# Optimization experiments

Measured on AMD Instinct MI355X. Metric: run time of the kernel, lower is better.

Reference implementation:

```python
import jax, jax.numpy as jnp
import numpy as np

N_NODES = 50000
N_EDGES = 600000
F_IN = 128
F_OUT = 128


def setup_inputs() -> dict:
    key = jax.random.key(0)
    k1, k2, k3, k4, k5 = jax.random.split(key, 5)
    x = jax.random.normal(k1, (N_NODES, F_IN), dtype=jnp.float32)
    src = jax.random.randint(k2, (N_EDGES,), 0, N_NODES)
    dst = jax.random.randint(k3, (N_EDGES,), 0, N_NODES)
    scale = 1.0 / np.sqrt(F_IN).astype(np.float32)
    W_self = jax.random.normal(k4, (F_IN, F_OUT), dtype=jnp.float32) * scale
    W_neigh = jax.random.normal(k5, (F_IN, F_OUT), dtype=jnp.float32) * scale
    b = jnp.zeros((F_OUT,), dtype=jnp.float32)
    return {"x": x, "W_self": W_self, "W_neigh": W_neigh, "b": b, "src": src, "dst": dst}


def reference(x, W_self, W_neigh, b, src, dst):
    # DGL SAGEConv, aggregator_type='mean':
    #   h_neigh[v] = mean_{(u->v) in E} x[u]   (0 for zero in-degree nodes)
    #   out = relu(x @ W_self + h_neigh @ W_neigh + b)
    msgs = x[src]  # [E, F_IN] gather of source features
    agg = jax.ops.segment_sum(msgs, dst, num_segments=N_NODES)  # [N, F_IN]
    deg = jax.ops.segment_sum(jnp.ones((src.shape[0],), x.dtype), dst,
                              num_segments=N_NODES)  # [N]
    h_neigh = agg / jnp.maximum(deg, 1.0)[:, None]  # zero-degree -> 0
    out = x @ W_self + h_neigh @ W_neigh + b
    return jax.nn.relu(out)
```

## Files before the change

### kernel.cpp

```cpp
#include <hip/hip_runtime.h>

#define F 128
#define HP 136
#define CAP 62
#define RSTR 64
#define PBASE ((int)0xAAAAAAAA)

typedef short bf16x8 __attribute__((ext_vector_type(8)));
typedef float f32x4  __attribute__((ext_vector_type(4)));

__device__ __forceinline__ unsigned short f2bf(float f) {
    unsigned int u = __float_as_uint(f);
    u += 0x7fffu + ((u >> 16) & 1u);
    return (unsigned short)(u >> 16);
}
__device__ __forceinline__ float bf2f(unsigned short s) {
    return __uint_as_float(((unsigned int)s) << 16);
}

__global__ __launch_bounds__(256) void build_kernel(
        const float* __restrict__ x, const float* __restrict__ Ws,
        const float* __restrict__ Wn,
        const int* __restrict__ src, const int* __restrict__ dst,
        unsigned short* __restrict__ xh, unsigned short* __restrict__ Bpack,
        unsigned short* __restrict__ rec, int n, int E) {
    int idx = blockIdx.x * 256 + threadIdx.x;

    bool has_x = idx < n * 16;
    float4 xv0, xv1;
    int node = idx >> 4;
    int xc = (idx & 15) * 8;
    if (has_x) {
        const float4* p = (const float4*)(x + (size_t)node * F + xc);
        xv0 = p[0];
        xv1 = p[1];
    }

    int e_d = 0, e_s = 0, e_p = CAP;
    if (idx < E) {
        e_d = dst[idx];
        e_s = src[idx];
        e_p = atomicAdd((int*)(rec + (size_t)e_d * RSTR), 1) - PBASE;
    }

    if (idx < 32768) {
        int j    = idx & 7;
        int lane = (idx >> 3) & 63;
        int tile = idx >> 9;
        int s = tile >> 3;
        int t = tile & 7;
        int k = s * 32 + (lane >> 4) * 8 + j;
        int c = t * 16 + (lane & 15);
        float v = (k < F) ? Ws[k * F + c] : Wn[(k - F) * F + c];
        Bpack[idx] = f2bf(v);
    }

    if (has_x) {
        bf16x8 o;
        o[0] = (short)f2bf(xv0.x); o[1] = (short)f2bf(xv0.y);
        o[2] = (short)f2bf(xv0.z); o[3] = (short)f2bf(xv0.w);
        o[4] = (short)f2bf(xv1.x); o[5] = (short)f2bf(xv1.y);
        o[6] = (short)f2bf(xv1.z); o[7] = (short)f2bf(xv1.w);
        *(bf16x8*)(xh + (size_t)node * F + xc) = o;
    }

    if (e_p < CAP)
        rec[(size_t)e_d * RSTR + 2 + e_p] = (unsigned short)e_s;
}

__global__ __launch_bounds__(256) void agg_gemm_kernel(
        const unsigned short* __restrict__ xh,
        const unsigned short* __restrict__ rec,
        const unsigned short* __restrict__ Bpack,
        const float* __restrict__ bias,
        float* __restrict__ out, int n) {
    __shared__ __align__(16) unsigned short hs[16 * HP];

    int tid = threadIdx.x;
    int r0 = blockIdx.x * 16;

    int l16 = tid & 15;
    int g = tid >> 4;
    int v = r0 + g;
    float acc[8] = {0.f, 0.f, 0.f, 0.f, 0.f, 0.f, 0.f, 0.f};
    if (v < n) {
        const unsigned short* rp = rec + (size_t)v * RSTR;
        int deg = *(const int*)rp - PBASE;
        int m = min(deg, CAP);
        const unsigned short* ep = rp + 2;
        int j = 0;
        for (; j + 4 <= m; j += 4) {
            int s0 = ep[j], s1 = ep[j + 1], s2 = ep[j + 2], s3 = ep[j + 3];
            bf16x8 v0 = *(const bf16x8*)(xh + (size_t)s0 * F + l16 * 8);
            bf16x8 v1 = *(const bf16x8*)(xh + (size_t)s1 * F + l16 * 8);
            bf16x8 v2 = *(const bf16x8*)(xh + (size_t)s2 * F + l16 * 8);
            bf16x8 v3 = *(const bf16x8*)(xh + (size_t)s3 * F + l16 * 8);
            #pragma unroll
            for (int i = 0; i < 8; ++i)
                acc[i] += (bf2f((unsigned short)v0[i]) + bf2f((unsigned short)v1[i]))
                        + (bf2f((unsigned short)v2[i]) + bf2f((unsigned short)v3[i]));
        }
        for (; j < m; ++j) {
            int s = ep[j];
            bf16x8 xv = *(const bf16x8*)(xh + (size_t)s * F + l16 * 8);
            #pragma unroll
            for (int i = 0; i < 8; ++i) acc[i] += bf2f((unsigned short)xv[i]);
        }
        float r = (deg > 0) ? 1.0f / (float)deg : 0.f;
        #pragma unroll
        for (int i = 0; i < 8; ++i) acc[i] *= r;
    }
    bf16x8 o;
    #pragma unroll
    for (int i = 0; i < 8; ++i) o[i] = (short)f2bf(acc[i]);
    *(bf16x8*)(&hs[g * HP + l16 * 8]) = o;
    __syncthreads();

    int wave = tid >> 6;
    int lane = tid & 63;
    int q = lane >> 4;
    int m = lane & 15;

    f32x4 acc2[2];
    acc2[0] = 0.f; acc2[1] = 0.f;

    int rA = min(r0 + m, n - 1);
    const unsigned short* ap = xh + (size_t)rA * F + q * 8;
    const unsigned short* hp = &hs[m * HP + q * 8];

    #pragma unroll
    for (int s = 0; s < 8; ++s) {
        bf16x8 a = (s < 4) ? *(const bf16x8*)(ap + s * 32)
                           : *(const bf16x8*)(hp + (s - 4) * 32);
        #pragma unroll
        for (int t = 0; t < 2; ++t) {
            bf16x8 bf = *(const bf16x8*)(Bpack + ((size_t)((s * 8 + wave * 2 + t) * 64 + lane)) * 8);
            acc2[t] = __builtin_amdgcn_mfma_f32_16x16x32_bf16(a, bf, acc2[t], 0, 0, 0);
        }
    }

    #pragma unroll
    for (int t = 0; t < 2; ++t) {
        int col = (wave * 2 + t) * 16 + m;
        float bv = bias[col];
        #pragma unroll
        for (int g2 = 0; g2 < 4; ++g2) {
            int row = r0 + q * 4 + g2;
            if (row < n)
                out[(size_t)row * F + col] = fmaxf(acc2[t][g2] + bv, 0.f);
        }
    }
}

extern "C" void kernel_launch(void* const* d_in, const int* in_sizes, int n_in,
                              void* d_out, int out_size, void* d_ws, size_t ws_size,
                              hipStream_t stream) {
    const float* x  = (const float*)d_in[0];
    const float* Ws = (const float*)d_in[1];
    const float* Wn = (const float*)d_in[2];
    const float* b  = (const float*)d_in[3];
    const int* src  = (const int*)d_in[4];
    const int* dst  = (const int*)d_in[5];
    int n = in_sizes[0] / F;
    int E = in_sizes[4];

    unsigned short* xh = (unsigned short*)d_ws;
    unsigned short* rec = xh + (size_t)n * F;
    unsigned short* Bpack = rec + (size_t)n * RSTR;

    float* out = (float*)d_out;

    build_kernel<<<(n * 16 + 255) / 256, 256, 0, stream>>>(x, Ws, Wn, src, dst,
                                                           xh, Bpack, rec, n, E);
    agg_gemm_kernel<<<(n + 15) / 16, 256, 0, stream>>>(xh, rec, Bpack, b, out, n);
}
```

Before: 152.0 us.

## Split bf16 features into four column planes and gather per plane

The bf16 copy of x is stored as four planes of 32 columns (64 bytes per node per plane) instead of one 256-byte row per node. The aggregation loops over the planes, and each thread gathers 4-byte words instead of 16-byte vectors, with software prefetching of the next group of four neighbours. The intent is to keep each plane (about 3.2MB) resident in cache while gathering and to cut register pressure, at the cost of re-reading the edge lists four times and issuing four times as many smaller loads.

```diff
diff --git a/kernel.cpp b/kernel.cpp
--- a/kernel.cpp
+++ b/kernel.cpp
@@ -14,9 +14,13 @@
     u += 0x7fffu + ((u >> 16) & 1u);
     return (unsigned short)(u >> 16);
 }
-__device__ __forceinline__ float bf2f(unsigned short s) {
-    return __uint_as_float(((unsigned int)s) << 16);
+__device__ __forceinline__ float bf2f_lo(unsigned int w) {
+    return __uint_as_float(w << 16);
 }
+__device__ __forceinline__ float bf2f_hi(unsigned int w) {
+    return __uint_as_float(w & 0xffff0000u);
+}
+
 
 __global__ __launch_bounds__(256) void build_kernel(
         const float* __restrict__ x, const float* __restrict__ Ws,
@@ -25,6 +29,7 @@
         unsigned short* __restrict__ xh, unsigned short* __restrict__ Bpack,
         unsigned short* __restrict__ rec, int n, int E) {
     int idx = blockIdx.x * 256 + threadIdx.x;
+    const size_t PL = (size_t)n * 32;
 
     bool has_x = idx < n * 16;
     float4 xv0, xv1;
@@ -61,7 +66,7 @@
         o[2] = (short)f2bf(xv0.z); o[3] = (short)f2bf(xv0.w);
         o[4] = (short)f2bf(xv1.x); o[5] = (short)f2bf(xv1.y);
         o[6] = (short)f2bf(xv1.z); o[7] = (short)f2bf(xv1.w);
-        *(bf16x8*)(xh + (size_t)node * F + xc) = o;
+        *(bf16x8*)(xh + (size_t)(xc >> 5) * PL + (size_t)node * 32 + (xc & 31)) = o;
     }
 
     if (e_p < CAP)
@@ -78,42 +83,58 @@
 
     int tid = threadIdx.x;
     int r0 = blockIdx.x * 16;
+    const size_t PL = (size_t)n * 32;
 
     int l16 = tid & 15;
     int g = tid >> 4;
     int v = r0 + g;
-    float acc[8] = {0.f, 0.f, 0.f, 0.f, 0.f, 0.f, 0.f, 0.f};
+    int deg = 0, mm = 0;
+    const unsigned short* ep = rec;
     if (v < n) {
         const unsigned short* rp = rec + (size_t)v * RSTR;
-        int deg = *(const int*)rp - PBASE;
-        int m = min(deg, CAP);
-        const unsigned short* ep = rp + 2;
+        deg = *(const int*)rp - PBASE;
+        mm = min(deg, CAP);
+        ep = rp + 2;
+    }
+    float r = (deg > 0) ? 1.0f / (float)deg : 0.f;
+
+    #pragma unroll
+    for (int q = 0; q < 4; ++q) {
+        const unsigned short* plane = xh + (size_t)q * PL;
+        float a0 = 0.f, a1 = 0.f;
         int j = 0;
-        for (; j + 4 <= m; j += 4) {
-            int s0 = ep[j], s1 = ep[j + 1], s2 = ep[j + 2], s3 = ep[j + 3];
-            bf16x8 v0 = *(const bf16x8*)(xh + (size_t)s0 * F + l16 * 8);
-            bf16x8 v1 = *(const bf16x8*)(xh + (size_t)s1 * F + l16 * 8);
-            bf16x8 v2 = *(const bf16x8*)(xh + (size_t)s2 * F + l16 * 8);
-            bf16x8 v3 = *(const bf16x8*)(xh + (size_t)s3 * F + l16 * 8);
-            #pragma unroll
-            for (int i = 0; i < 8; ++i)
-                acc[i] += (bf2f((unsigned short)v0[i]) + bf2f((unsigned short)v1[i]))
-                        + (bf2f((unsigned short)v2[i]) + bf2f((unsigned short)v3[i]));
+        if (mm >= 4) {
+            unsigned int s01 = *(const unsigned int*)(ep);
+            unsigned int s23 = *(const unsigned int*)(ep + 2);
+            unsigned int A0 = *(const unsigned int*)(plane + (size_t)(s01 & 0xffffu) * 32 + l16 * 2);
+            unsigned int A1 = *(const unsigned int*)(plane + (size_t)(s01 >> 16) * 32 + l16 * 2);
+            unsigned int A2 = *(const unsigned int*)(plane + (size_t)(s23 & 0xffffu) * 32 + l16 * 2);
+            unsigned int A3 = *(const unsigned int*)(plane + (size_t)(s23 >> 16) * 32 + l16 * 2);
+            j = 4;
+            while (j + 4 <= mm) {
+                unsigned int t01 = *(const unsigned int*)(ep + j);
+                unsigned int t23 = *(const unsigned int*)(ep + j + 2);
+                unsigned int B0 = *(const unsigned int*)(plane + (size_t)(t01 & 0xffffu) * 32 + l16 * 2);
+                unsigned int B1 = *(const unsigned int*)(plane + (size_t)(t01 >> 16) * 32 + l16 * 2);
+                unsigned int B2 = *(const unsigned int*)(plane + (size_t)(t23 & 0xffffu) * 32 + l16 * 2);
+                unsigned int B3 = *(const unsigned int*)(plane + (size_t)(t23 >> 16) * 32 + l16 * 2);
+                a0 += (bf2f_lo(A0) + bf2f_lo(A1)) + (bf2f_lo(A2) + bf2f_lo(A3));
+                a1 += (bf2f_hi(A0) + bf2f_hi(A1)) + (bf2f_hi(A2) + bf2f_hi(A3));
+                A0 = B0; A1 = B1; A2 = B2; A3 = B3;
+                j += 4;
+            }
+            a0 += (bf2f_lo(A0) + bf2f_lo(A1)) + (bf2f_lo(A2) + bf2f_lo(A3));
+            a1 += (bf2f_hi(A0) + bf2f_hi(A1)) + (bf2f_hi(A2) + bf2f_hi(A3));
         }
-        for (; j < m; ++j) {
-            int s = ep[j];
-            bf16x8 xv = *(const bf16x8*)(xh + (size_t)s * F + l16 * 8);
-            #pragma unroll
-            for (int i = 0; i < 8; ++i) acc[i] += bf2f((unsigned short)xv[i]);
+        for (; j < mm; ++j) {
+            unsigned int w = *(const unsigned int*)(plane + (size_t)ep[j] * 32 + l16 * 2);
+            a0 += bf2f_lo(w);
+            a1 += bf2f_hi(w);
         }
-        float r = (deg > 0) ? 1.0f / (float)deg : 0.f;
-        #pragma unroll
-        for (int i = 0; i < 8; ++i) acc[i] *= r;
+        a0 *= r; a1 *= r;
+        unsigned int packed = (unsigned int)f2bf(a0) | ((unsigned int)f2bf(a1) << 16);
+        *(unsigned int*)(&hs[g * HP + q * 32 + l16 * 2]) = packed;
     }
-    bf16x8 o;
-    #pragma unroll
-    for (int i = 0; i < 8; ++i) o[i] = (short)f2bf(acc[i]);
-    *(bf16x8*)(&hs[g * HP + l16 * 8]) = o;
     __syncthreads();
 
     int wave = tid >> 6;
@@ -125,12 +146,11 @@
     acc2[0] = 0.f; acc2[1] = 0.f;
 
     int rA = min(r0 + m, n - 1);
-    const unsigned short* ap = xh + (size_t)rA * F + q * 8;
     const unsigned short* hp = &hs[m * HP + q * 8];
 
     #pragma unroll
     for (int s = 0; s < 8; ++s) {
-        bf16x8 a = (s < 4) ? *(const bf16x8*)(ap + s * 32)
+        bf16x8 a = (s < 4) ? *(const bf16x8*)(xh + (size_t)s * PL + (size_t)rA * 32 + q * 8)
                            : *(const bf16x8*)(hp + (s - 4) * 32);
         #pragma unroll
         for (int t = 0; t < 2; ++t) {
```

New measurement: 172.5 us. +13.5%, slower.
